# Performance work log

Hardware: AMD Instinct MI355X
Metric: run time of the kernel (lower is better)

The kernel has to match this reference:

```python
import jax, jax.numpy as jnp
import numpy as np

HEADS = 8
D_MODEL = 512
D_K = D_MODEL // HEADS
B, S = 2, 2048


def setup_inputs() -> dict:
    key = jax.random.key(0)
    ks = jax.random.split(key, 12)
    f = lambda k, shape: jax.random.normal(k, shape, dtype=jnp.float32)
    inp = {
        'q': f(ks[0], (B, S, D_MODEL)),
        'k': f(ks[1], (B, S, D_MODEL)),
        'v': f(ks[2], (B, S, D_MODEL)),
        'mask': jax.random.randint(ks[3], (B, S, S), 0, 2, dtype=jnp.int32),
        'Wq': f(ks[4], (D_MODEL, D_MODEL)) * 0.02,
        'bq': jnp.zeros((D_MODEL,), jnp.float32),
        'Wk': f(ks[5], (D_MODEL, D_MODEL)) * 0.02,
        'bk': jnp.zeros((D_MODEL,), jnp.float32),
        'Wv': f(ks[6], (D_MODEL, D_MODEL)) * 0.02,
        'bv': jnp.zeros((D_MODEL,), jnp.float32),
        'Wo': f(ks[7], (D_MODEL, D_MODEL)) * 0.02,
        'bo': jnp.zeros((D_MODEL,), jnp.float32),
    }
    return inp


def reference(q, k, v, mask, Wq, bq, Wk, bk, Wv, bv, Wo, bo):
    bs = q.shape[0]
    # linear projections then split heads: [B, H, S, D_K]
    qh = (q @ Wq + bq).reshape(bs, -1, HEADS, D_K).transpose(0, 2, 1, 3)
    kh = (k @ Wk + bk).reshape(bs, -1, HEADS, D_K).transpose(0, 2, 1, 3)
    vh = (v @ Wv + bv).reshape(bs, -1, HEADS, D_K).transpose(0, 2, 1, 3)
    # scores: [B, H, Sq, Sk]
    scores = jnp.einsum('bhqd,bhkd->bhqk', qh, kh) / jnp.sqrt(jnp.float32(D_K))
    scores = jnp.where(mask[:, None, :, :] == 0, jnp.float32(-10000.0), scores)
    attn = jax.nn.softmax(scores, axis=-1)
    # dropout p=0.0 -> identity (inference-equivalent)
    ctx = jnp.einsum('bhqk,bhkd->bhqd', attn, vh)
    concat = ctx.transpose(0, 2, 1, 3).reshape(bs, -1, D_MODEL)
    out = concat @ Wo + bo
    return (out, attn)
```

## Files before the change

kernel.cpp:

```cpp
#include <hip/hip_runtime.h>
#include <math.h>

#define HEADS 8
#define DK 64
#define DMODEL 512
#define BATCH 2
#define SEQ 2048
#define BH (BATCH * HEADS)

using f32x4 = __attribute__((ext_vector_type(4))) float;
using s16x8 = __attribute__((ext_vector_type(8))) short;
using fp16x2 = __attribute__((ext_vector_type(2))) __fp16;

union FragU {
  uint4 u;
  s16x8 s;
  unsigned short us[8];
};
union PkU {
  fp16x2 h;
  unsigned int u;
};

__device__ __forceinline__ unsigned short f32_to_bf16(float f) {
  unsigned int u = __float_as_uint(f);
  u += 0x7fffu + ((u >> 16) & 1u);
  return (unsigned short)(u >> 16);
}
__device__ __forceinline__ float bf16_to_f32(unsigned short h) {
  return __uint_as_float(((unsigned int)h) << 16);
}

__global__ __launch_bounds__(256) void wsplit4_kernel(
    const float* __restrict__ W0, const float* __restrict__ W1,
    const float* __restrict__ W2, const float* __restrict__ W3,
    unsigned short* __restrict__ WtHi4, unsigned short* __restrict__ WtLo4) {
  __shared__ float t[64][65];
  const int z = blockIdx.z;
  const float* W = (z == 0) ? W0 : (z == 1) ? W1 : (z == 2) ? W2 : W3;
  unsigned short* WtHi = WtHi4 + (size_t)z * (DMODEL * DMODEL);
  unsigned short* WtLo = WtLo4 + (size_t)z * (DMODEL * DMODEL);
  const int k0 = blockIdx.x * 64, n0 = blockIdx.y * 64;
  const int tid = threadIdx.x;
  const int r = tid >> 2, c = (tid & 3) * 16;
  #pragma unroll
  for (int e = 0; e < 4; ++e) {
    f32x4 v = *(const f32x4*)&W[(size_t)(k0 + r) * DMODEL + n0 + c + e * 4];
    #pragma unroll
    for (int j = 0; j < 4; ++j) t[r][c + e * 4 + j] = v[j];
  }
  __syncthreads();
  const int rn = tid >> 2, ck = (tid & 3) * 16;
  #pragma unroll
  for (int half = 0; half < 2; ++half) {
    FragU hi, lo;
    #pragma unroll
    for (int e = 0; e < 8; ++e) {
      float x = t[ck + half * 8 + e][rn];
      unsigned short h = f32_to_bf16(x);
      hi.us[e] = h;
      lo.us[e] = f32_to_bf16(x - bf16_to_f32(h));
    }
    const size_t o = (size_t)(n0 + rn) * DMODEL + k0 + ck + half * 8;
    *(uint4*)&WtHi[o] = hi.u;
    *(uint4*)&WtLo[o] = lo.u;
  }
}

__global__ __launch_bounds__(256) void fused_front_kernel(
    const float* __restrict__ Xq, const float* __restrict__ Xk,
    const float* __restrict__ Xv, const unsigned short* __restrict__ WtHi4,
    const unsigned short* __restrict__ WtLo4, const float* __restrict__ bq,
    const float* __restrict__ bk, const float* __restrict__ bv,
    unsigned short* __restrict__ Qhi, unsigned short* __restrict__ Qlo,
    unsigned short* __restrict__ Khi, unsigned short* __restrict__ Vt,
    const int* __restrict__ mask, unsigned int* __restrict__ bits) {
  __shared__ unsigned short BsHi[64][72];
  __shared__ unsigned short BsLo[64][72];
  const int id = blockIdx.x;
  const int tid = threadIdx.x;

  if (id >= 1536) {
    const int row = id - 1536;
    const int4* mrow = (const int4*)&mask[(size_t)row * SEQ + tid * 8];
    const int4 a = mrow[0];
    const int4 bb = mrow[1];
    unsigned int byte = 0;
    byte |= (a.x != 0) ? 1u : 0u;
    byte |= (a.y != 0) ? 2u : 0u;
    byte |= (a.z != 0) ? 4u : 0u;
    byte |= (a.w != 0) ? 8u : 0u;
    byte |= (bb.x != 0) ? 16u : 0u;
    byte |= (bb.y != 0) ? 32u : 0u;
    byte |= (bb.z != 0) ? 64u : 0u;
    byte |= (bb.w != 0) ? 128u : 0u;
    ((unsigned char*)bits)[(size_t)row * 256 + tid] = (unsigned char)byte;
    return;
  }

  const int z = id >> 9;
  const int rem = id & 511;
  const int m0 = (rem & 63) * 64;
  const int n0 = (rem >> 6) * 64;
  const float* X = (z == 0) ? Xq : (z == 1) ? Xk : Xv;
  const float* bias = (z == 0) ? bq : (z == 1) ? bk : bv;
  const unsigned short* WtHi = WtHi4 + (size_t)z * (DMODEL * DMODEL);
  const unsigned short* WtLo = WtLo4 + (size_t)z * (DMODEL * DMODEL);

  const int wv = tid >> 6, lane = tid & 63;
  const int lr = lane & 15, lg = lane >> 4;
  const int mw = m0 + wv * 16;

  f32x4 acc[4] = {};
  for (int k0 = 0; k0 < 512; k0 += 64) {
    FragU ah[2], al[2];
    #pragma unroll
    for (int dc = 0; dc < 2; ++dc) {
      const size_t xi = (size_t)(mw + lr) * DMODEL + k0 + dc * 32 + lg * 8;
      f32x4 x0 = *(const f32x4*)&X[xi];
      f32x4 x1 = *(const f32x4*)&X[xi + 4];
      #pragma unroll
      for (int t = 0; t < 4; ++t) {
        unsigned short h0 = f32_to_bf16(x0[t]);
        unsigned short h1 = f32_to_bf16(x1[t]);
        ah[dc].us[t] = h0;
        ah[dc].us[4 + t] = h1;
        al[dc].us[t] = f32_to_bf16(x0[t] - bf16_to_f32(h0));
        al[dc].us[4 + t] = f32_to_bf16(x1[t] - bf16_to_f32(h1));
      }
    }
    __syncthreads();
    #pragma unroll
    for (int e = 0; e < 2; ++e) {
      const int rr = (tid >> 3) + e * 32;
      const int cc = (tid & 7) * 8;
      *(uint4*)&BsHi[rr][cc] =
          *(const uint4*)&WtHi[(size_t)(n0 + rr) * DMODEL + k0 + cc];
      *(uint4*)&BsLo[rr][cc] =
          *(const uint4*)&WtLo[(size_t)(n0 + rr) * DMODEL + k0 + cc];
    }
    __syncthreads();
    #pragma unroll
    for (int jt = 0; jt < 4; ++jt) {
      #pragma unroll
      for (int dc = 0; dc < 2; ++dc) {
        FragU bh, bl;
        bh.u = *(const uint4*)&BsHi[jt * 16 + lr][dc * 32 + lg * 8];
        bl.u = *(const uint4*)&BsLo[jt * 16 + lr][dc * 32 + lg * 8];
        acc[jt] = __builtin_amdgcn_mfma_f32_16x16x32_bf16(ah[dc].s, bh.s, acc[jt], 0, 0, 0);
        acc[jt] = __builtin_amdgcn_mfma_f32_16x16x32_bf16(ah[dc].s, bl.s, acc[jt], 0, 0, 0);
        acc[jt] = __builtin_amdgcn_mfma_f32_16x16x32_bf16(al[dc].s, bh.s, acc[jt], 0, 0, 0);
      }
    }
  }

  __syncthreads();
  #pragma unroll
  for (int jt = 0; jt < 4; ++jt) {
    const int n = jt * 16 + lr;
    const float bi = bias[n0 + n];
    #pragma unroll
    for (int r = 0; r < 4; ++r) {
      const float v = acc[jt][r] + bi;
      const int row = wv * 16 + lg * 4 + r;
      unsigned short hi = f32_to_bf16(v);
      BsHi[row][n] = hi;
      if (z == 0) BsLo[row][n] = f32_to_bf16(v - bf16_to_f32(hi));
    }
  }
  __syncthreads();
  if (z == 2) {
    const int b2 = m0 >> 11, s0 = m0 & 2047, hh = n0 >> 6;
    const int d = tid >> 2, sc = (tid & 3) * 16;
    #pragma unroll
    for (int e = 0; e < 16; ++e)
      Vt[((size_t)(b2 * HEADS + hh) * DK + d) * SEQ + s0 + sc + e] =
          BsHi[sc + e][d];
  } else {
    unsigned short* Yhi = (z == 0) ? Qhi : Khi;
    #pragma unroll
    for (int p = 0; p < 2; ++p) {
      const int row = (tid >> 3) + p * 32;
      const int ch = (tid & 7) * 8;
      const size_t o = (size_t)(m0 + row) * DMODEL + n0 + ch;
      *(uint4*)&Yhi[o] = *(uint4*)&BsHi[row][ch];
      if (z == 0) *(uint4*)&Qlo[o] = *(uint4*)&BsLo[row][ch];
    }
  }
}

__global__ __launch_bounds__(256) void proj_out_kernel(
    const unsigned short* __restrict__ X16, const unsigned short* __restrict__ WtHi,
    const unsigned short* __restrict__ WtLo, const float* __restrict__ bias,
    float* __restrict__ Yf) {
  __shared__ unsigned short BsHi[64][72];
  __shared__ unsigned short BsLo[64][72];
  const int tid = threadIdx.x, wv = tid >> 6, lane = tid & 63;
  const int lr = lane & 15, lg = lane >> 4;
  const int m0 = blockIdx.x * 64;
  const int mw = m0 + wv * 16;
  const int n0 = blockIdx.y * 64;

  f32x4 acc[4] = {};
  for (int k0 = 0; k0 < 512; k0 += 64) {
    FragU ah[2];
    #pragma unroll
    for (int dc = 0; dc < 2; ++dc) {
      const size_t xi = (size_t)(mw + lr) * DMODEL + k0 + dc * 32 + lg * 8;
      ah[dc].u = *(const uint4*)&X16[xi];
    }
    __syncthreads();
    #pragma unroll
    for (int e = 0; e < 2; ++e) {
      const int rr = (tid >> 3) + e * 32;
      const int cc = (tid & 7) * 8;
      *(uint4*)&BsHi[rr][cc] =
          *(const uint4*)&WtHi[(size_t)(n0 + rr) * DMODEL + k0 + cc];
      *(uint4*)&BsLo[rr][cc] =
          *(const uint4*)&WtLo[(size_t)(n0 + rr) * DMODEL + k0 + cc];
    }
    __syncthreads();
    #pragma unroll
    for (int jt = 0; jt < 4; ++jt) {
      #pragma unroll
      for (int dc = 0; dc < 2; ++dc) {
        FragU bh, bl;
        bh.u = *(const uint4*)&BsHi[jt * 16 + lr][dc * 32 + lg * 8];
        bl.u = *(const uint4*)&BsLo[jt * 16 + lr][dc * 32 + lg * 8];
        acc[jt] = __builtin_amdgcn_mfma_f32_16x16x32_bf16(ah[dc].s, bh.s, acc[jt], 0, 0, 0);
        acc[jt] = __builtin_amdgcn_mfma_f32_16x16x32_bf16(ah[dc].s, bl.s, acc[jt], 0, 0, 0);
      }
    }
  }
  #pragma unroll
  for (int jt = 0; jt < 4; ++jt) {
    const int n = n0 + jt * 16 + lr;
    const float bi = bias[n];
    #pragma unroll
    for (int r = 0; r < 4; ++r)
      Yf[(size_t)(mw + lg * 4 + r) * DMODEL + n] = acc[jt][r] + bi;
  }
}

__global__ __launch_bounds__(1024) void attn_fused_kernel(
    const unsigned short* __restrict__ Qhi, const unsigned short* __restrict__ Qlo,
    const unsigned short* __restrict__ Khi, const unsigned int* __restrict__ bits,
    const unsigned short* __restrict__ Vt, float* __restrict__ attn,
    unsigned short* __restrict__ ctx16) {
  __shared__ unsigned short pbuf[16][16 * 76];
  __shared__ float smred[16][16];
  const int id = blockIdx.x;
  const int xcd = id & 7, slot = id >> 3;
  const int bh = xcd + 8 * (slot & 1);
  const int qt = slot >> 1;
  const int b = bh >> 3, h = bh & 7;
  const int tid = threadIdx.x, wv = tid >> 6, lane = tid & 63;
  const int lr = lane & 15, lg = lane >> 4;
  const int q0 = qt * 16;
  const int kw = wv * 128;

  FragU qh[2], ql[2];
  #pragma unroll
  for (int dc = 0; dc < 2; ++dc) {
    const size_t qi = (size_t)(b * SEQ + q0 + lr) * DMODEL + h * DK + dc * 32 + lg * 8;
    qh[dc].u = *(const uint4*)&Qhi[qi];
    ql[dc].u = *(const uint4*)&Qlo[qi];
  }
  uint4 mw4[4];
  #pragma unroll
  for (int r = 0; r < 4; ++r) {
    const int q = q0 + lg * 4 + r;
    mw4[r] = *(const uint4*)&bits[((size_t)b * SEQ + q) * 64 + (kw >> 5)];
  }

  const float C = 0.125f * 1.44269504089f;
  PkU epk[8][2];
  float ls[4] = {0.f, 0.f, 0.f, 0.f};
  #pragma unroll
  for (int t = 0; t < 8; ++t) {
    FragU kh[2];
    #pragma unroll
    for (int dc = 0; dc < 2; ++dc) {
      const size_t kidx =
          (size_t)(b * SEQ + kw + t * 16 + lr) * DMODEL + h * DK + dc * 32 + lg * 8;
      kh[dc].u = *(const uint4*)&Khi[kidx];
    }
    f32x4 sa = {};
    #pragma unroll
    for (int dc = 0; dc < 2; ++dc) {
      sa = __builtin_amdgcn_mfma_f32_16x16x32_bf16(qh[dc].s, kh[dc].s, sa, 0, 0, 0);
      sa = __builtin_amdgcn_mfma_f32_16x16x32_bf16(ql[dc].s, kh[dc].s, sa, 0, 0, 0);
    }
    float ev[4];
    #pragma unroll
    for (int r = 0; r < 4; ++r) {
      const unsigned int w =
          (t >> 1) == 0 ? mw4[r].x : (t >> 1) == 1 ? mw4[r].y
          : (t >> 1) == 2 ? mw4[r].z : mw4[r].w;
      const bool keep = (w >> (((t & 1) << 4) + lr)) & 1;
      const float e = keep ? exp2f(sa[r] * C) : 0.0f;
      ev[r] = e;
      ls[r] += e;
    }
    epk[t][0].h = __builtin_amdgcn_cvt_pkrtz(ev[0], ev[1]);
    epk[t][1].h = __builtin_amdgcn_cvt_pkrtz(ev[2], ev[3]);
  }

  #pragma unroll
  for (int r = 0; r < 4; ++r) {
    #pragma unroll
    for (int off = 1; off < 16; off <<= 1) ls[r] += __shfl_xor(ls[r], off);
    if (lr == 0) smred[wv][lg * 4 + r] = ls[r];
  }
  __syncthreads();
  float il[4];
  #pragma unroll
  for (int r = 0; r < 4; ++r) {
    float l = 0.f;
    #pragma unroll
    for (int w2 = 0; w2 < 16; ++w2) l += smred[w2][lg * 4 + r];
    il[r] = 1.0f / l;
  }

  unsigned short* pb = pbuf[wv];
  f32x4 acc[4] = {};
  #pragma unroll
  for (int c = 0; c < 2; ++c) {
    #pragma unroll
    for (int tt = 0; tt < 4; ++tt) {
      const int t = c * 4 + tt;
      float pv4[4];
      pv4[0] = (float)epk[t][0].h.x * il[0];
      pv4[1] = (float)epk[t][0].h.y * il[1];
      pv4[2] = (float)epk[t][1].h.x * il[2];
      pv4[3] = (float)epk[t][1].h.y * il[3];
      #pragma unroll
      for (int r = 0; r < 4; ++r) {
        const int q = q0 + lg * 4 + r;
        attn[((size_t)bh * SEQ + q) * SEQ + kw + t * 16 + lr] = pv4[r];
        pb[(lg * 4 + r) * 76 + tt * 16 + lr] = f32_to_bf16(pv4[r]);
      }
    }
    #pragma unroll
    for (int dc2 = 0; dc2 < 2; ++dc2) {
      FragU pa;
      pa.u = *(const uint4*)&pb[lr * 76 + dc2 * 32 + lg * 8];
      #pragma unroll
      for (int dt = 0; dt < 4; ++dt) {
        FragU bv;
        bv.u = *(const uint4*)&Vt[((size_t)bh * DK + dt * 16 + lr) * SEQ + kw +
                                  c * 64 + dc2 * 32 + lg * 8];
        acc[dt] = __builtin_amdgcn_mfma_f32_16x16x32_bf16(pa.s, bv.s, acc[dt], 0, 0, 0);
      }
    }
  }

  float* red = (float*)&pbuf[0][0];
  #pragma unroll 1
  for (int ofs = 8; ofs > 0; ofs >>= 1) {
    __syncthreads();
    if (wv >= ofs && wv < 2 * ofs) {
      float* dst = red + (size_t)(wv - ofs) * 1024;
      #pragma unroll
      for (int dt = 0; dt < 4; ++dt) *(f32x4*)&dst[dt * 256 + lane * 4] = acc[dt];
    }
    __syncthreads();
    if (wv < ofs) {
      const float* src = red + (size_t)wv * 1024;
      #pragma unroll
      for (int dt = 0; dt < 4; ++dt) acc[dt] += *(const f32x4*)&src[dt * 256 + lane * 4];
    }
  }
  if (wv == 0) {
    #pragma unroll
    for (int dt = 0; dt < 4; ++dt)
      #pragma unroll
      for (int r = 0; r < 4; ++r) {
        const int q = q0 + lg * 4 + r;
        ctx16[(size_t)(b * SEQ + q) * DMODEL + h * DK + dt * 16 + lr] =
            f32_to_bf16(acc[dt][r]);
      }
  }
}

extern "C" void kernel_launch(void* const* d_in, const int* in_sizes, int n_in,
                              void* d_out, int out_size, void* d_ws,
                              size_t ws_size, hipStream_t stream) {
  const float* q = (const float*)d_in[0];
  const float* k = (const float*)d_in[1];
  const float* v = (const float*)d_in[2];
  const int* mask = (const int*)d_in[3];
  const float* Wq = (const float*)d_in[4];
  const float* bq = (const float*)d_in[5];
  const float* Wk = (const float*)d_in[6];
  const float* bk = (const float*)d_in[7];
  const float* Wv = (const float*)d_in[8];
  const float* bv = (const float*)d_in[9];
  const float* Wo = (const float*)d_in[10];
  const float* bo = (const float*)d_in[11];

  float* out = (float*)d_out;
  float* attn = out + (size_t)BATCH * SEQ * DMODEL;

  char* w = (char*)d_ws;
  const size_t MB = 1u << 20;
  unsigned short* Qhi = (unsigned short*)(w + 0 * MB);
  unsigned short* Qlo = (unsigned short*)(w + 4 * MB);
  unsigned short* Khi = (unsigned short*)(w + 8 * MB);
  unsigned short* WtHi4 = (unsigned short*)(w + 12 * MB);
  unsigned short* WtLo4 = (unsigned short*)(w + 14 * MB);
  unsigned short* ctx16 = (unsigned short*)(w + 16 * MB);
  unsigned short* Vt = (unsigned short*)(w + 20 * MB);
  unsigned int* bits = (unsigned int*)(w + 24 * MB);

  const size_t WSTRIDE = (size_t)DMODEL * DMODEL;

  dim3 blk(256);
  wsplit4_kernel<<<dim3(8, 8, 4), blk, 0, stream>>>(Wq, Wk, Wv, Wo, WtHi4, WtLo4);

  fused_front_kernel<<<dim3(5632), blk, 0, stream>>>(
      q, k, v, WtHi4, WtLo4, bq, bk, bv, Qhi, Qlo, Khi, Vt, mask, bits);

  attn_fused_kernel<<<dim3(2048), dim3(1024), 0, stream>>>(Qhi, Qlo, Khi, bits,
                                                           Vt, attn, ctx16);

  proj_out_kernel<<<dim3(64, 8), blk, 0, stream>>>(
      ctx16, WtHi4 + 3 * WSTRIDE, WtLo4 + 3 * WSTRIDE, bo, out);
}
```

Baseline: 239.0 us.

## Halve attention block to 8 waves with 256 keys per wave and batched loads

The attention kernel now runs 512 threads (8 waves) per block instead of 1024, so each wave covers 256 keys instead of 128. The cross-wave reduction loses one level. K fragments are loaded in batches of 8 tiles before the MFMAs, and V fragments are loaded ahead of each P·V chunk, to give more memory-level parallelism per wave. The cost is more registers per wave (epk grows to 16 entries, plus kh and vv buffers), which may lower occupancy or cause spills.

```diff
diff --git a/kernel.cpp b/kernel.cpp
--- a/kernel.cpp
+++ b/kernel.cpp
@@ -242,13 +242,13 @@
   }
 }
 
-__global__ __launch_bounds__(1024) void attn_fused_kernel(
+__global__ __launch_bounds__(512) void attn_fused_kernel(
     const unsigned short* __restrict__ Qhi, const unsigned short* __restrict__ Qlo,
     const unsigned short* __restrict__ Khi, const unsigned int* __restrict__ bits,
     const unsigned short* __restrict__ Vt, float* __restrict__ attn,
     unsigned short* __restrict__ ctx16) {
-  __shared__ unsigned short pbuf[16][16 * 76];
-  __shared__ float smred[16][16];
+  __shared__ unsigned short pbuf[8][16 * 76];
+  __shared__ float smred[8][16];
   const int id = blockIdx.x;
   const int xcd = id & 7, slot = id >> 3;
   const int bh = xcd + 8 * (slot & 1);
@@ -257,7 +257,7 @@
   const int tid = threadIdx.x, wv = tid >> 6, lane = tid & 63;
   const int lr = lane & 15, lg = lane >> 4;
   const int q0 = qt * 16;
-  const int kw = wv * 128;
+  const int kw = wv * 256;
 
   FragU qh[2], ql[2];
   #pragma unroll
@@ -266,44 +266,54 @@
     qh[dc].u = *(const uint4*)&Qhi[qi];
     ql[dc].u = *(const uint4*)&Qlo[qi];
   }
-  uint4 mw4[4];
+  uint4 mw8[4][2];
   #pragma unroll
   for (int r = 0; r < 4; ++r) {
-    const int q = q0 + lg * 4 + r;
-    mw4[r] = *(const uint4*)&bits[((size_t)b * SEQ + q) * 64 + (kw >> 5)];
+    const size_t base = ((size_t)b * SEQ + q0 + lg * 4 + r) * 64 + (kw >> 5);
+    mw8[r][0] = *(const uint4*)&bits[base];
+    mw8[r][1] = *(const uint4*)&bits[base + 4];
   }
 
   const float C = 0.125f * 1.44269504089f;
-  PkU epk[8][2];
+  PkU epk[16][2];
   float ls[4] = {0.f, 0.f, 0.f, 0.f};
   #pragma unroll
-  for (int t = 0; t < 8; ++t) {
-    FragU kh[2];
-    #pragma unroll
-    for (int dc = 0; dc < 2; ++dc) {
-      const size_t kidx =
-          (size_t)(b * SEQ + kw + t * 16 + lr) * DMODEL + h * DK + dc * 32 + lg * 8;
-      kh[dc].u = *(const uint4*)&Khi[kidx];
-    }
-    f32x4 sa = {};
-    #pragma unroll
-    for (int dc = 0; dc < 2; ++dc) {
-      sa = __builtin_amdgcn_mfma_f32_16x16x32_bf16(qh[dc].s, kh[dc].s, sa, 0, 0, 0);
-      sa = __builtin_amdgcn_mfma_f32_16x16x32_bf16(ql[dc].s, kh[dc].s, sa, 0, 0, 0);
-    }
-    float ev[4];
-    #pragma unroll
-    for (int r = 0; r < 4; ++r) {
-      const unsigned int w =
-          (t >> 1) == 0 ? mw4[r].x : (t >> 1) == 1 ? mw4[r].y
-          : (t >> 1) == 2 ? mw4[r].z : mw4[r].w;
-      const bool keep = (w >> (((t & 1) << 4) + lr)) & 1;
-      const float e = keep ? exp2f(sa[r] * C) : 0.0f;
-      ev[r] = e;
-      ls[r] += e;
-    }
-    epk[t][0].h = __builtin_amdgcn_cvt_pkrtz(ev[0], ev[1]);
-    epk[t][1].h = __builtin_amdgcn_cvt_pkrtz(ev[2], ev[3]);
+  for (int g = 0; g < 2; ++g) {
+    FragU kh[8][2];
+    #pragma unroll
+    for (int tt = 0; tt < 8; ++tt) {
+      const int t = g * 8 + tt;
+      #pragma unroll
+      for (int dc = 0; dc < 2; ++dc) {
+        const size_t kidx =
+            (size_t)(b * SEQ + kw + t * 16 + lr) * DMODEL + h * DK + dc * 32 + lg * 8;
+        kh[tt][dc].u = *(const uint4*)&Khi[kidx];
+      }
+    }
+    #pragma unroll
+    for (int tt = 0; tt < 8; ++tt) {
+      const int t = g * 8 + tt;
+      f32x4 sa = {};
+      #pragma unroll
+      for (int dc = 0; dc < 2; ++dc) {
+        sa = __builtin_amdgcn_mfma_f32_16x16x32_bf16(qh[dc].s, kh[tt][dc].s, sa, 0, 0, 0);
+        sa = __builtin_amdgcn_mfma_f32_16x16x32_bf16(ql[dc].s, kh[tt][dc].s, sa, 0, 0, 0);
+      }
+      const int wi = t >> 1;
+      float ev[4];
+      #pragma unroll
+      for (int r = 0; r < 4; ++r) {
+        const uint4 m4 = mw8[r][wi >> 2];
+        const unsigned int w =
+            (wi & 3) == 0 ? m4.x : (wi & 3) == 1 ? m4.y : (wi & 3) == 2 ? m4.z : m4.w;
+        const bool keep = (w >> (((t & 1) << 4) + lr)) & 1;
+        const float e = keep ? exp2f(sa[r] * C) : 0.0f;
+        ev[r] = e;
+        ls[r] += e;
+      }
+      epk[t][0].h = __builtin_amdgcn_cvt_pkrtz(ev[0], ev[1]);
+      epk[t][1].h = __builtin_amdgcn_cvt_pkrtz(ev[2], ev[3]);
+    }
   }
 
   #pragma unroll
@@ -318,14 +328,21 @@
   for (int r = 0; r < 4; ++r) {
     float l = 0.f;
     #pragma unroll
-    for (int w2 = 0; w2 < 16; ++w2) l += smred[w2][lg * 4 + r];
+    for (int w2 = 0; w2 < 8; ++w2) l += smred[w2][lg * 4 + r];
     il[r] = 1.0f / l;
   }
 
   unsigned short* pb = pbuf[wv];
   f32x4 acc[4] = {};
   #pragma unroll
-  for (int c = 0; c < 2; ++c) {
+  for (int c = 0; c < 4; ++c) {
+    FragU vv[2][4];
+    #pragma unroll
+    for (int dc2 = 0; dc2 < 2; ++dc2)
+      #pragma unroll
+      for (int dt = 0; dt < 4; ++dt)
+        vv[dc2][dt].u = *(const uint4*)&Vt[((size_t)bh * DK + dt * 16 + lr) * SEQ +
+                                           kw + c * 64 + dc2 * 32 + lg * 8];
     #pragma unroll
     for (int tt = 0; tt < 4; ++tt) {
       const int t = c * 4 + tt;
@@ -346,18 +363,14 @@
       FragU pa;
       pa.u = *(const uint4*)&pb[lr * 76 + dc2 * 32 + lg * 8];
       #pragma unroll
-      for (int dt = 0; dt < 4; ++dt) {
-        FragU bv;
-        bv.u = *(const uint4*)&Vt[((size_t)bh * DK + dt * 16 + lr) * SEQ + kw +
-                                  c * 64 + dc2 * 32 + lg * 8];
-        acc[dt] = __builtin_amdgcn_mfma_f32_16x16x32_bf16(pa.s, bv.s, acc[dt], 0, 0, 0);
-      }
+      for (int dt = 0; dt < 4; ++dt)
+        acc[dt] = __builtin_amdgcn_mfma_f32_16x16x32_bf16(pa.s, vv[dc2][dt].s, acc[dt], 0, 0, 0);
     }
   }
 
   float* red = (float*)&pbuf[0][0];
   #pragma unroll 1
-  for (int ofs = 8; ofs > 0; ofs >>= 1) {
+  for (int ofs = 4; ofs > 0; ofs >>= 1) {
     __syncthreads();
     if (wv >= ofs && wv < 2 * ofs) {
       float* dst = red + (size_t)(wv - ofs) * 1024;
@@ -421,8 +434,8 @@
   fused_front_kernel<<<dim3(5632), blk, 0, stream>>>(
       q, k, v, WtHi4, WtLo4, bq, bk, bv, Qhi, Qlo, Khi, Vt, mask, bits);
 
-  attn_fused_kernel<<<dim3(2048), dim3(1024), 0, stream>>>(Qhi, Qlo, Khi, bits,
-                                                           Vt, attn, ctx16);
+  attn_fused_kernel<<<dim3(2048), dim3(512), 0, stream>>>(Qhi, Qlo, Khi, bits,
+                                                          Vt, attn, ctx16);
 
   proj_out_kernel<<<dim3(64, 8), blk, 0, stream>>>(
       ctx16, WtHi4 + 3 * WSTRIDE, WtLo4 + 3 * WSTRIDE, bo, out);
```

Result: faster. 208.5 us, median of 2 (-12.8%).
